# Kernel tuning notes

Measured on AMD Instinct MI355X. Metric: run time of the kernel, lower is better.

The kernel has to match this reference:

```python
import jax, jax.numpy as jnp
import numpy as np

L1, L2, L3, COUNT, B = 3072, 15, 32, 8, 16384

def setup_inputs() -> dict:
    key = jax.random.key(0)
    ks = jax.random.split(key, 10)
    s = 1.0 / np.sqrt(L1)
    inp = {
        'x': jax.random.normal(ks[0], (B, L1), dtype=jnp.float32),
        'ls_indices': jax.random.randint(ks[1], (B,), 0, COUNT, dtype=jnp.int64 if jax.config.jax_enable_x64 else jnp.int32),
        # l1: Linear(L1, (L2+1)*count)
        'l1_w': jax.random.uniform(ks[2], ((L2 + 1) * COUNT, L1), jnp.float32, -s, s),
        'l1_b': jax.random.uniform(ks[3], ((L2 + 1) * COUNT,), jnp.float32, -s, s),
        # l1_fact: Linear(L1, L2+1) -- zero-initialized in the original module
        'l1f_w': jnp.zeros((L2 + 1, L1), jnp.float32),
        'l1f_b': jnp.zeros((L2 + 1,), jnp.float32),
        # l2: Linear(2*L2, L3*count)
        'l2_w': jax.random.uniform(ks[4], (L3 * COUNT, 2 * L2), jnp.float32, -0.18, 0.18),
        'l2_b': jax.random.uniform(ks[5], (L3 * COUNT,), jnp.float32, -0.18, 0.18),
        # output: Linear(L3, count) -- bias zero-initialized
        'out_w': jax.random.uniform(ks[6], (COUNT, L3), jnp.float32, -0.176, 0.176),
        'out_b': jnp.zeros((COUNT,), jnp.float32),
    }
    return inp

def reference(x, ls_indices, l1_w, l1_b, l1f_w, l1f_b, l2_w, l2_b, out_w, out_b):
    Bn = x.shape[0]
    rows = jnp.arange(Bn)
    idx = ls_indices.astype(jnp.int32)

    # l1: compute all stacks, gather selected
    l1s = (x @ l1_w.T + l1_b).reshape(Bn, COUNT, L2 + 1)   # [B, count, 16]
    l1c = l1s[rows, idx]                                    # [B, 16]
    l1f = x @ l1f_w.T + l1f_b                               # [B, 16]
    l1c_main, l1c_out = l1c[:, :L2], l1c[:, L2:]            # [B,15],[B,1]
    l1f_main, l1f_out = l1f[:, :L2], l1f[:, L2:]

    l1x = l1c_main + l1f_main                               # [B, 15]
    l1x = jnp.clip(jnp.concatenate([jnp.square(l1x) * (127.0 / 128.0), l1x], axis=1), 0.0, 1.0)  # [B, 30]

    # l2
    l2s = (l1x @ l2_w.T + l2_b).reshape(Bn, COUNT, L3)      # [B, count, 32]
    l2x = jnp.clip(l2s[rows, idx], 0.0, 1.0)                # [B, 32]

    # output
    l3s = l2x @ out_w.T + out_b                             # [B, count]
    l3c = l3s[rows, idx][:, None]                           # [B, 1]
    return l3c + l1f_out + l1c_out                          # [B, 1]
```

## Files before the change

kernel.cpp:

```cpp
#include <hip/hip_runtime.h>
#include <hip/hip_bf16.h>

#define BATCH 16384
#define K1DIM 3072
#define NCOUNT 8
#define NO 16

typedef float f32x4 __attribute__((ext_vector_type(4)));

__host__ __device__ constexpr int brev6(int i) {
    int r = 0;
    for (int b = 0; b < 6; ++b) r |= ((i >> b) & 1) << (5 - b);
    return r;
}

__global__ __launch_bounds__(256) void k_combine(const float* __restrict__ l1w,
                                                 const float* __restrict__ l1fw,
                                                 float* __restrict__ wc) {
    int i = blockIdx.x * 256 + threadIdx.x;
    int row = i / 768;
    int col = (i - row * 768) * 4;
    int o = row & 15;
    f32x4 a = *(const f32x4*)(l1w + (size_t)row * K1DIM + col);
    f32x4 f = *(const f32x4*)(l1fw + (size_t)o * K1DIM + col);
    *(f32x4*)(wc + (size_t)row * K1DIM + col) = a + f;
}

__global__ __launch_bounds__(256) void k_bucket(const int* __restrict__ ls,
                                                int* __restrict__ counts,
                                                int* __restrict__ bucketArr) {
    __shared__ int h[NCOUNT];
    __shared__ int hbase[NCOUNT];
    int t = threadIdx.x;
    if (t < NCOUNT) h[t] = 0;
    __syncthreads();
    int i = blockIdx.x * 256 + t;
    int idx = ls[i];
    int lpos = atomicAdd(&h[idx], 1);
    __syncthreads();
    if (t < NCOUNT) hbase[t] = atomicAdd(&counts[t], h[t]);
    __syncthreads();
    bucketArr[idx * BATCH + hbase[idx] + lpos] = i;
}

__global__ void k_sched(const int* __restrict__ counts, int* __restrict__ blkoff) {
    if (threadIdx.x == 0) {
        int acc = 0;
        for (int i = 0; i < NCOUNT; ++i) {
            blkoff[i] = acc;
            acc += (counts[i] + 15) >> 4;
        }
        blkoff[NCOUNT] = acc;
    }
}

__global__ __launch_bounds__(256) void k_gemm(
    const float* __restrict__ x, const float* __restrict__ wc_all,
    const float* __restrict__ l1b, const float* __restrict__ l1fb,
    const int* __restrict__ bucketArr, const int* __restrict__ counts,
    const int* __restrict__ blkoff, float* __restrict__ y) {
    int b = blockIdx.x;
    if (b >= blkoff[NCOUNT]) return;
    int bucket = 0;
#pragma unroll
    for (int i = 1; i < NCOUNT; ++i)
        if (b >= blkoff[i]) bucket = i;
    int chunk = b - blkoff[bucket];
    int count = counts[bucket];

    int t = threadIdx.x;
    int lane = t & 63;
    int wid = t >> 6;

    const int* bk = bucketArr + bucket * BATCH;
    int base = chunk * 16 + wid * 4;
    int g0 = min(base + 0, count - 1);
    int g1 = min(base + 1, count - 1);
    int g2 = min(base + 2, count - 1);
    int g3 = min(base + 3, count - 1);
    int sid0 = bk[g0], sid1 = bk[g1], sid2 = bk[g2], sid3 = bk[g3];
    const float* xr0 = x + (size_t)sid0 * K1DIM + lane * 4;
    const float* xr1 = x + (size_t)sid1 * K1DIM + lane * 4;
    const float* xr2 = x + (size_t)sid2 * K1DIM + lane * 4;
    const float* xr3 = x + (size_t)sid3 * K1DIM + lane * 4;
    const float* wp = wc_all + (size_t)bucket * NO * K1DIM + lane * 4;

    float acc[64];
#pragma unroll
    for (int i = 0; i < 64; ++i) acc[i] = 0.f;

#pragma unroll 2
    for (int it = 0; it < K1DIM / 256; ++it) {
        int k = it * 256;
        f32x4 xv0 = __builtin_nontemporal_load((const f32x4*)(xr0 + k));
        f32x4 xv1 = __builtin_nontemporal_load((const f32x4*)(xr1 + k));
        f32x4 xv2 = __builtin_nontemporal_load((const f32x4*)(xr2 + k));
        f32x4 xv3 = __builtin_nontemporal_load((const f32x4*)(xr3 + k));
#pragma unroll
        for (int o = 0; o < NO; ++o) {
            f32x4 wv = *(const f32x4*)(wp + o * K1DIM + k);
#define ACCUM(S, XV)                                                     \
            {                                                            \
                float& a_ = acc[brev6((S)*16 + o)];                      \
                a_ = fmaf(XV.x, wv.x, a_);                               \
                a_ = fmaf(XV.y, wv.y, a_);                               \
                a_ = fmaf(XV.z, wv.z, a_);                               \
                a_ = fmaf(XV.w, wv.w, a_);                               \
            }
            ACCUM(0, xv0) ACCUM(1, xv1) ACCUM(2, xv2) ACCUM(3, xv3)
#undef ACCUM
        }
    }

#pragma unroll
    for (int st = 0; st < 6; ++st) {
        const int m = 1 << st;
        const int half = 32 >> st;
        const bool hi = (lane & m) != 0;
#pragma unroll
        for (int i = 0; i < half; ++i) {
            float mine = hi ? acc[i] : acc[i + half];
            float other = __shfl_xor(mine, m, 64);
            float keep = hi ? acc[i + half] : acc[i];
            acc[i] = keep + other;
        }
    }

    int p_s = lane >> 4;
    int p_o = lane & 15;
    int gp = min(base + p_s, count - 1);
    int sid = bk[gp];
    float bias = l1b[bucket * NO + p_o] + l1fb[p_o];
    y[(size_t)sid * NO + p_o] = acc[0] + bias;
}

__global__ __launch_bounds__(256) void k_tail(
    const float* __restrict__ y, const int* __restrict__ ls,
    const float* __restrict__ l2w, const float* __restrict__ l2b,
    const float* __restrict__ outw, const float* __restrict__ outb,
    float* __restrict__ out) {
    int gt = blockIdx.x * 256 + threadIdx.x;
    int s = gt >> 5;
    int o2 = gt & 31;
    int idx = ls[s];
    const f32x4* yp = (const f32x4*)(y + (size_t)s * NO);
    f32x4 a0 = yp[0], a1 = yp[1], a2 = yp[2], a3 = yp[3];
    float v[16] = {a0.x, a0.y, a0.z, a0.w, a1.x, a1.y, a1.z, a1.w,
                   a2.x, a2.y, a2.z, a2.w, a3.x, a3.y, a3.z, a3.w};
    float l1x[30];
#pragma unroll
    for (int j = 0; j < 15; ++j) {
        float tv = v[j];
        float sq = tv * tv * (127.f / 128.f);
        l1x[j] = fminf(fmaxf(sq, 0.f), 1.f);
        l1x[j + 15] = fminf(fmaxf(tv, 0.f), 1.f);
    }
    const float* wr = l2w + (size_t)idx * 32 * 30 + o2 * 30;
    float tacc = l2b[idx * 32 + o2];
#pragma unroll
    for (int j = 0; j < 15; ++j) {
        float2 wpv = *(const float2*)(wr + j * 2);
        tacc = fmaf(l1x[j * 2], wpv.x, tacc);
        tacc = fmaf(l1x[j * 2 + 1], wpv.y, tacc);
    }
    tacc = fminf(fmaxf(tacc, 0.f), 1.f);
    float r = tacc * outw[idx * 32 + o2];
#pragma unroll
    for (int m = 1; m < 32; m <<= 1) r += __shfl_xor(r, m, 64);
    if (o2 == 0) out[s] = r + outb[idx] + v[15];
}

extern "C" void kernel_launch(void* const* d_in, const int* in_sizes, int n_in,
                              void* d_out, int out_size, void* d_ws, size_t ws_size,
                              hipStream_t stream) {
    const float* x    = (const float*)d_in[0];
    const int*   ls   = (const int*)  d_in[1];
    const float* l1w  = (const float*)d_in[2];
    const float* l1b  = (const float*)d_in[3];
    const float* l1fw = (const float*)d_in[4];
    const float* l1fb = (const float*)d_in[5];
    const float* l2w  = (const float*)d_in[6];
    const float* l2b  = (const float*)d_in[7];
    const float* outw = (const float*)d_in[8];
    const float* outb = (const float*)d_in[9];
    float* out = (float*)d_out;

    char* ws = (char*)d_ws;
    float* wc       = (float*)ws;
    float* y        = (float*)(ws + 1572864);
    int*   bucketArr= (int*)(ws + 1572864 + 1048576);
    int*   counts   = (int*)(ws + 1572864 + 1048576 + 524288);
    int*   blkoff   = (int*)(ws + 1572864 + 1048576 + 524288 + 64);

    (void)hipMemsetAsync(counts, 0, 64, stream);
    k_combine<<<384, 256, 0, stream>>>(l1w, l1fw, wc);
    k_bucket<<<BATCH / 256, 256, 0, stream>>>(ls, counts, bucketArr);
    k_sched<<<1, 64, 0, stream>>>(counts, blkoff);
    k_gemm<<<1031, 256, 0, stream>>>(x, wc, l1b, l1fb,
                                     bucketArr, counts, blkoff, y);
    k_tail<<<BATCH * 32 / 256, 256, 0, stream>>>(y, ls, l2w, l2b, outw, outb, out);
}
```

Before: 384.2 us.

## Stage weights via double-buffered LDS, halve rows per wave, inline block scheduling

Weight chunks for each bucket are now loaded into a double-buffered LDS tile with global_load_lds, and all four waves read them from there instead of each wave fetching weights from global memory. Each wave now handles 2 samples instead of 4, so accumulators drop from 64 to 32 and launch bounds request higher occupancy. The grid doubles to 2055 blocks, and the block-offset scheduling is computed inline in each block, which removes the k_sched launch. The costs are a __syncthreads per K chunk, an extra cross-half shuffle reduction, and half the lanes idle during the store.

```diff
diff --git a/kernel.cpp b/kernel.cpp
--- a/kernel.cpp
+++ b/kernel.cpp
@@ -5,12 +5,15 @@
 #define K1DIM 3072
 #define NCOUNT 8
 #define NO 16
+#define CHUNK 256
+#define NCHUNK (K1DIM / CHUNK)
 
 typedef float f32x4 __attribute__((ext_vector_type(4)));
-
-__host__ __device__ constexpr int brev6(int i) {
+typedef unsigned int u32;
+
+__host__ __device__ constexpr int brev5(int i) {
     int r = 0;
-    for (int b = 0; b < 6; ++b) r |= ((i >> b) & 1) << (5 - b);
+    for (int b = 0; b < 5; ++b) r |= ((i >> b) & 1) << (4 - b);
     return r;
 }
 
@@ -43,79 +46,96 @@
     bucketArr[idx * BATCH + hbase[idx] + lpos] = i;
 }
 
-__global__ void k_sched(const int* __restrict__ counts, int* __restrict__ blkoff) {
-    if (threadIdx.x == 0) {
-        int acc = 0;
-        for (int i = 0; i < NCOUNT; ++i) {
-            blkoff[i] = acc;
-            acc += (counts[i] + 15) >> 4;
-        }
-        blkoff[NCOUNT] = acc;
-    }
-}
-
-__global__ __launch_bounds__(256) void k_gemm(
+__device__ __forceinline__ void stage4(const float* gbase, float* lds_linear,
+                                       int wid, int lane) {
+#pragma unroll
+    for (int i = 0; i < 4; ++i) {
+        int row = wid * 4 + i;
+        const float* g = gbase + (size_t)row * K1DIM + lane * 4;
+        float* l = lds_linear + row * CHUNK;
+        __builtin_amdgcn_global_load_lds(
+            (const __attribute__((address_space(1))) u32*)g,
+            (__attribute__((address_space(3))) u32*)l, 16, 0, 0);
+    }
+}
+
+__global__ __launch_bounds__(256, 5) void k_gemm(
     const float* __restrict__ x, const float* __restrict__ wc_all,
     const float* __restrict__ l1b, const float* __restrict__ l1fb,
     const int* __restrict__ bucketArr, const int* __restrict__ counts,
-    const int* __restrict__ blkoff, float* __restrict__ y) {
+    float* __restrict__ y) {
+    __shared__ float buf[2][NO * CHUNK];
+
+    int cnt[NCOUNT], off[NCOUNT];
+    int nblk = 0;
+#pragma unroll
+    for (int i = 0; i < NCOUNT; ++i) {
+        cnt[i] = counts[i];
+        off[i] = nblk;
+        nblk += (cnt[i] + 7) >> 3;
+    }
     int b = blockIdx.x;
-    if (b >= blkoff[NCOUNT]) return;
+    if (b >= nblk) return;
     int bucket = 0;
 #pragma unroll
-    for (int i = 1; i < NCOUNT; ++i)
-        if (b >= blkoff[i]) bucket = i;
-    int chunk = b - blkoff[bucket];
-    int count = counts[bucket];
+    for (int i = 1; i < NCOUNT; ++i) if (b >= off[i]) bucket = i;
+    int chunkblk = b - off[bucket];
+    int count = cnt[bucket];
 
     int t = threadIdx.x;
     int lane = t & 63;
     int wid = t >> 6;
 
     const int* bk = bucketArr + bucket * BATCH;
-    int base = chunk * 16 + wid * 4;
+    int base = chunkblk * 8 + wid * 2;
     int g0 = min(base + 0, count - 1);
     int g1 = min(base + 1, count - 1);
-    int g2 = min(base + 2, count - 1);
-    int g3 = min(base + 3, count - 1);
-    int sid0 = bk[g0], sid1 = bk[g1], sid2 = bk[g2], sid3 = bk[g3];
+    int sid0 = bk[g0], sid1 = bk[g1];
     const float* xr0 = x + (size_t)sid0 * K1DIM + lane * 4;
     const float* xr1 = x + (size_t)sid1 * K1DIM + lane * 4;
-    const float* xr2 = x + (size_t)sid2 * K1DIM + lane * 4;
-    const float* xr3 = x + (size_t)sid3 * K1DIM + lane * 4;
-    const float* wp = wc_all + (size_t)bucket * NO * K1DIM + lane * 4;
-
-    float acc[64];
-#pragma unroll
-    for (int i = 0; i < 64; ++i) acc[i] = 0.f;
-
-#pragma unroll 2
-    for (int it = 0; it < K1DIM / 256; ++it) {
-        int k = it * 256;
+    const float* wstack = wc_all + (size_t)bucket * NO * K1DIM;
+
+    float acc[32];
+#pragma unroll
+    for (int i = 0; i < 32; ++i) acc[i] = 0.f;
+
+    stage4(wstack, &buf[0][0], wid, lane);
+
+    for (int it = 0; it < NCHUNK; ++it) {
+        int cur = it & 1;
+        __syncthreads();
+        if (it + 1 < NCHUNK)
+            stage4(wstack + (it + 1) * CHUNK, &buf[cur ^ 1][0], wid, lane);
+        int k = it * CHUNK;
         f32x4 xv0 = __builtin_nontemporal_load((const f32x4*)(xr0 + k));
         f32x4 xv1 = __builtin_nontemporal_load((const f32x4*)(xr1 + k));
-        f32x4 xv2 = __builtin_nontemporal_load((const f32x4*)(xr2 + k));
-        f32x4 xv3 = __builtin_nontemporal_load((const f32x4*)(xr3 + k));
+        const float* lb = &buf[cur][lane * 4];
 #pragma unroll
         for (int o = 0; o < NO; ++o) {
-            f32x4 wv = *(const f32x4*)(wp + o * K1DIM + k);
-#define ACCUM(S, XV)                                                     \
-            {                                                            \
-                float& a_ = acc[brev6((S)*16 + o)];                      \
-                a_ = fmaf(XV.x, wv.x, a_);                               \
-                a_ = fmaf(XV.y, wv.y, a_);                               \
-                a_ = fmaf(XV.z, wv.z, a_);                               \
-                a_ = fmaf(XV.w, wv.w, a_);                               \
+            f32x4 wv = *(const f32x4*)(lb + o * CHUNK);
+            {
+                float& a_ = acc[brev5(o)];
+                a_ = fmaf(xv0.x, wv.x, a_);
+                a_ = fmaf(xv0.y, wv.y, a_);
+                a_ = fmaf(xv0.z, wv.z, a_);
+                a_ = fmaf(xv0.w, wv.w, a_);
             }
-            ACCUM(0, xv0) ACCUM(1, xv1) ACCUM(2, xv2) ACCUM(3, xv3)
-#undef ACCUM
+            {
+                float& a_ = acc[brev5(16 + o)];
+                a_ = fmaf(xv1.x, wv.x, a_);
+                a_ = fmaf(xv1.y, wv.y, a_);
+                a_ = fmaf(xv1.z, wv.z, a_);
+                a_ = fmaf(xv1.w, wv.w, a_);
+            }
         }
     }
 
 #pragma unroll
-    for (int st = 0; st < 6; ++st) {
+    for (int i = 0; i < 32; ++i) acc[i] += __shfl_xor(acc[i], 32, 64);
+#pragma unroll
+    for (int st = 0; st < 5; ++st) {
         const int m = 1 << st;
-        const int half = 32 >> st;
+        const int half = 16 >> st;
         const bool hi = (lane & m) != 0;
 #pragma unroll
         for (int i = 0; i < half; ++i) {
@@ -126,12 +146,14 @@
         }
     }
 
-    int p_s = lane >> 4;
-    int p_o = lane & 15;
-    int gp = min(base + p_s, count - 1);
-    int sid = bk[gp];
-    float bias = l1b[bucket * NO + p_o] + l1fb[p_o];
-    y[(size_t)sid * NO + p_o] = acc[0] + bias;
+    if (lane < 32) {
+        int p_s = lane >> 4;
+        int p_o = lane & 15;
+        int gp = min(base + p_s, count - 1);
+        int sid = bk[gp];
+        float bias = l1b[bucket * NO + p_o] + l1fb[p_o];
+        y[(size_t)sid * NO + p_o] = acc[0] + bias;
+    }
 }
 
 __global__ __launch_bounds__(256) void k_tail(
@@ -190,13 +212,10 @@
     float* y        = (float*)(ws + 1572864);
     int*   bucketArr= (int*)(ws + 1572864 + 1048576);
     int*   counts   = (int*)(ws + 1572864 + 1048576 + 524288);
-    int*   blkoff   = (int*)(ws + 1572864 + 1048576 + 524288 + 64);
-
-    (void)hipMemsetAsync(counts, 0, 64, stream);
+
+    (void)hipMemsetAsync(counts, 0, 32, stream);
     k_combine<<<384, 256, 0, stream>>>(l1w, l1fw, wc);
     k_bucket<<<BATCH / 256, 256, 0, stream>>>(ls, counts, bucketArr);
-    k_sched<<<1, 64, 0, stream>>>(counts, blkoff);
-    k_gemm<<<1031, 256, 0, stream>>>(x, wc, l1b, l1fb,
-                                     bucketArr, counts, blkoff, y);
+    k_gemm<<<2055, 256, 0, stream>>>(x, wc, l1b, l1fb, bucketArr, counts, y);
     k_tail<<<BATCH * 32 / 256, 256, 0, stream>>>(y, ls, l2w, l2b, outw, outb, out);
 }
```

New measurement: 351.9 us. 8.4% less time.
